# Performance work log

Measured on AMD Instinct MI355X. Metric: run time of the kernel, lower is better.

## Reference

```python
import jax, jax.numpy as jnp
import numpy as np

N = 100_000            # nodes
E = 1_600_000          # edges per metapath
IN = 256               # input features
HEADS, DIM = 8, 16     # heads * dim = hidden_channels
HIDDEN = HEADS * DIM   # 128
OUT = 4                # classes
NEG_SLOPE = 0.2


def setup_inputs() -> dict:
    key = jax.random.key(0)
    ks = jax.random.split(key, 16)
    s = 1.0 / np.sqrt(HIDDEN)
    return {
        "x": jax.random.normal(ks[0], (N, IN), jnp.float32),
        "edge_index0": jax.random.randint(ks[1], (2, E), 0, N, jnp.int64),
        "edge_index1": jax.random.randint(ks[2], (2, E), 0, N, jnp.int64),
        "proj_w": jax.random.normal(ks[3], (IN, HIDDEN), jnp.float32) / np.sqrt(IN),
        "proj_b": jnp.zeros((HIDDEN,), jnp.float32),
        "att_src0": jax.random.normal(ks[4], (HEADS, DIM), jnp.float32) * s,
        "att_dst0": jax.random.normal(ks[5], (HEADS, DIM), jnp.float32) * s,
        "att_src1": jax.random.normal(ks[6], (HEADS, DIM), jnp.float32) * s,
        "att_dst1": jax.random.normal(ks[7], (HEADS, DIM), jnp.float32) * s,
        "k_lin_w": jax.random.normal(ks[8], (HIDDEN, HIDDEN), jnp.float32) * s,
        "k_lin_b": jnp.zeros((HIDDEN,), jnp.float32),
        "q": jax.random.normal(ks[9], (HIDDEN,), jnp.float32) * s,
        "lin_w": jax.random.normal(ks[10], (HIDDEN, OUT), jnp.float32) * s,
        "lin_b": jnp.zeros((OUT,), jnp.float32),
    }


def _metapath_conv(xp, a_src, a_dst, src, dst):
    # xp: [N,H,D]; a_src, a_dst: [H,D]; src/dst: [E]
    alpha_src = (xp * a_src).sum(-1)                     # [N,H]
    alpha_dst = (xp * a_dst).sum(-1)                     # [N,H]
    e = jax.nn.leaky_relu(alpha_src[src] + alpha_dst[dst], NEG_SLOPE)  # [E,H]
    emax = jax.ops.segment_max(e, dst, num_segments=N)  # [N,H] (stable softmax)
    e = jnp.exp(e - emax[dst])
    denom = jax.ops.segment_sum(e, dst, num_segments=N)
    alpha = e / (denom[dst] + 1e-16)                     # edge softmax per dst
    msg = xp[src] * alpha[..., None]                     # [E,H,D]
    out = jax.ops.segment_sum(msg, dst, num_segments=N)  # [N,H,D]
    return jax.nn.relu(out.reshape(N, HIDDEN))


def reference(x, edge_index0, edge_index1, proj_w, proj_b,
              att_src0, att_dst0, att_src1, att_dst1,
              k_lin_w, k_lin_b, q, lin_w, lin_b):
    # shared node-type projection
    xp = (x @ proj_w + proj_b).reshape(N, HEADS, DIM)
    # per-metapath GAT-style convolutions (dropout=0.6 is eval no-op)
    outs = jnp.stack([
        _metapath_conv(xp, att_src0, att_dst0, edge_index0[0], edge_index0[1]),
        _metapath_conv(xp, att_src1, att_dst1, edge_index1[0], edge_index1[1]),
    ])                                                    # [M,N,HIDDEN]
    # semantic attention over metapaths
    k = jnp.tanh(outs @ k_lin_w + k_lin_b).mean(axis=1)  # [M,HIDDEN]
    attn = jax.nn.softmax((k * q).sum(-1))               # [M]
    fused = (attn[:, None, None] * outs).sum(0)          # [N,HIDDEN]
    return fused @ lin_w + lin_b                          # [N,OUT]
```

## Files before the change

kernel.cpp:

```cpp
#include <hip/hip_runtime.h>
#include <hip/hip_bf16.h>

#define NN 100000
#define EE 1600000
#define HID 128
#define NEG 0.2f
#define CAP 64
#define BSH 9
#define NB 196
#define CAPB 9216
#define EBLK 4096
#define NBINB 391
#define NBUILD 392
#define NPROJ 512

typedef __attribute__((ext_vector_type(8))) short short8;
typedef __attribute__((ext_vector_type(4))) float f32x4;

static __device__ __forceinline__ float bf2f(short s) {
  union { float f; unsigned u; } c;
  c.u = ((unsigned)(unsigned short)s) << 16;
  return c.f;
}

static __device__ __forceinline__ float exp2_fast(float x) {
  float r;
  asm("v_exp_f32 %0, %1" : "=v"(r) : "v"(x));
  return r;
}

static __device__ __forceinline__ float tanh_fast(float x) {
  float a = fminf(fmaxf(x * 2.885390082f, -40.f), 40.f);
  float e = exp2_fast(a);
  float r = __builtin_amdgcn_rcpf(e + 1.f);
  return fmaf(-2.f, r, 1.f);
}

__global__ __launch_bounds__(256) void k_prep(const int* __restrict__ ei0,
    const int* __restrict__ ei1, const float* __restrict__ w,
    const float* __restrict__ kw, int* __restrict__ gcur,
    int* __restrict__ binned, short* __restrict__ wTg, short* __restrict__ kwTg) {
  const int bid = blockIdx.x;
  const int t = threadIdx.x;
  if (bid >= 2 * NBINB) {
    int i = (bid - 2 * NBINB) * 256 + t;
    if (i < 32768) {
      int n = i >> 8, k = i & 255;
      __hip_bfloat16 b = __float2bfloat16(w[k * 128 + n]);
      wTg[i] = *(short*)&b;
    } else if (i < 49152) {
      int j = i - 32768;
      int n = j >> 7, k = j & 127;
      __hip_bfloat16 b = __float2bfloat16(kw[k * 128 + n]);
      kwTg[j] = *(short*)&b;
    }
    return;
  }
  const int p = bid >= NBINB;
  const int bx = p ? bid - NBINB : bid;
  const int* __restrict__ ei = p ? ei1 : ei0;
  const int* __restrict__ src = ei;
  const int* __restrict__ dst = ei + EE;
  int* __restrict__ gc = gcur + p * 256;
  int* __restrict__ bn = binned + (size_t)p * NB * CAPB;
  __shared__ int cntL[NB], baseL[NB];
  const int e0 = bx * EBLK;
  const int e1 = min(e0 + EBLK, EE);
  for (int i = t; i < NB; i += 256) cntL[i] = 0;
  __syncthreads();
  int vj[16], bj[16];
#pragma unroll
  for (int j = 0; j < 16; j++) {
    int e = e0 + t + j * 256;
    bj[j] = -1;
    if (e < e1) {
      int d = dst[e];
      int b = d >> BSH;
      int off = atomicAdd(&cntL[b], 1);
      vj[j] = (src[e] << BSH) | (d & 511);
      bj[j] = (b << 14) | off;
    }
  }
  __syncthreads();
  for (int i = t; i < NB; i += 256) baseL[i] = atomicAdd(&gc[i], cntL[i]);
  __syncthreads();
#pragma unroll
  for (int j = 0; j < 16; j++) {
    if (bj[j] >= 0) {
      int b = bj[j] >> 14;
      int off = baseL[b] + (bj[j] & 16383);
      if (off < CAPB) bn[b * CAPB + off] = vj[j];
    }
  }
}

#define PWS 264
#define PNT ((NN + 15) / 16)

__global__ __launch_bounds__(512) void k_mid(
    const int* __restrict__ gcur, const int* __restrict__ binned,
    int* __restrict__ cnt, int* __restrict__ csr,
    const float* __restrict__ x, const short* __restrict__ wTg,
    const float* __restrict__ bias,
    const float* __restrict__ a0s, const float* __restrict__ a0d,
    const float* __restrict__ a1s, const float* __restrict__ a1d,
    __hip_bfloat16* __restrict__ xph,
    float* __restrict__ as0, float* __restrict__ ad0,
    float* __restrict__ as1, float* __restrict__ ad1) {
  __shared__ short wT[128 * PWS];
  const int bid = blockIdx.x;
  const int tid = threadIdx.x;
  if (bid < NBUILD) {
    int* lc = (int*)wT;
    const int p = bid >= 196, b = p ? bid - 196 : bid;
    const int* __restrict__ bn = binned + (size_t)p * NB * CAPB + (size_t)b * CAPB;
    const int n = min(gcur[p * 256 + b], CAPB);
    int* __restrict__ cs = csr + (size_t)p * NN * CAP;
    lc[tid] = 0;
    __syncthreads();
    const int node0 = b << BSH;
    for (int i = tid; i < n; i += 512) {
      int v = bn[i];
      int ln = v & 511;
      int off = atomicAdd(&lc[ln], 1);
      if (off < CAP) cs[(size_t)(node0 + ln) * CAP + off] = v >> BSH;
    }
    __syncthreads();
    int n0 = node0 + tid;
    if (n0 < NN) cnt[p * NN + n0] = lc[tid];
    return;
  }
  const int pb = bid - NBUILD;
  for (int i = tid; i < 4096; i += 512) {
    int n = i >> 5, kc = i & 31;
    *(short8*)&wT[n * PWS + kc * 8] = *(const short8*)&wTg[n * 256 + kc * 8];
  }
  const int lane = tid & 63, wave = tid >> 6;
  const int rowgrp = lane >> 4, lcol = lane & 15;
  const bool b3 = (lcol & 8) != 0, b2 = (lcol & 4) != 0;
  const int ttype = (lcol >> 2) & 3;
  float* __restrict__ ap = (ttype == 0) ? as0 : (ttype == 1) ? ad0
                         : (ttype == 2) ? as1 : ad1;
  float bv[8], AS0[8], AD0[8], AS1[8], AD1[8];
  const float L2E = 1.44269504f;
#pragma unroll
  for (int ct = 0; ct < 8; ct++) {
    bv[ct] = bias[ct * 16 + lcol];
    AS0[ct] = a0s[ct * 16 + lcol] * L2E;
    AD0[ct] = a0d[ct * 16 + lcol] * L2E;
    AS1[ct] = a1s[ct * 16 + lcol] * L2E;
    AD1[ct] = a1d[ct * 16 + lcol] * L2E;
  }
  __syncthreads();
  for (int tile = pb * 8 + wave; tile < PNT; tile += NPROJ * 8) {
    const int r0 = tile * 16;
    int row = r0 + lcol;
    if (row >= NN) row = NN - 1;
    const float* xr = x + (size_t)row * 256 + rowgrp * 8;
    short8 af[8];
#pragma unroll
    for (int kc = 0; kc < 8; kc++) {
      float4 u0 = *(const float4*)(xr + kc * 32);
      float4 u1 = *(const float4*)(xr + kc * 32 + 4);
      union { short8 v; __hip_bfloat162 h[4]; } u;
      u.h[0] = __float22bfloat162_rn(make_float2(u0.x, u0.y));
      u.h[1] = __float22bfloat162_rn(make_float2(u0.z, u0.w));
      u.h[2] = __float22bfloat162_rn(make_float2(u1.x, u1.y));
      u.h[3] = __float22bfloat162_rn(make_float2(u1.z, u1.w));
      af[kc] = u.v;
    }
#pragma unroll
    for (int ct = 0; ct < 8; ct++) {
      f32x4 acc = {0.f, 0.f, 0.f, 0.f};
#pragma unroll
      for (int kc = 0; kc < 8; kc++) {
        short8 bf = *(const short8*)&wT[(ct * 16 + lcol) * PWS + kc * 32 + rowgrp * 8];
        acc = __builtin_amdgcn_mfma_f32_16x16x32_bf16(af[kc], bf, acc, 0, 0, 0);
      }
#pragma unroll
      for (int r = 0; r < 4; r++) {
        int orow = r0 + rowgrp * 4 + r;
        float xv = acc[r] + bv[ct];
        if (orow < NN) {
          __hip_bfloat16 ob = __float2bfloat16(xv);
          ((short*)xph)[(size_t)orow * 128 + ct * 16 + lcol] = *(short*)&ob;
        }
        float q0 = xv * AS0[ct], q1 = xv * AD0[ct], q2 = xv * AS1[ct], q3 = xv * AD1[ct];
        float va = (b3 ? q2 : q0) + __shfl_xor(b3 ? q0 : q2, 8, 64);
        float vb = (b3 ? q3 : q1) + __shfl_xor(b3 ? q1 : q3, 8, 64);
        float v  = (b2 ? vb : va) + __shfl_xor(b2 ? va : vb, 4, 64);
        v += __shfl_xor(v, 2, 64);
        v += __shfl_xor(v, 1, 64);
        if ((lcol & 3) == 0 && orow < NN) ap[orow * 8 + ct] = v;
      }
    }
  }
}


#define EDGE_BODY(sv)                                      \
  {                                                        \
    unsigned s = (unsigned)(sv);                           \
    float t = asrc[s * 8u + h];                            \
    __hip_bfloat162 v = xph[s * 64u + lane];               \
    float tt = t + ad;                                     \
    float al = exp2_fast(fmaxf(tt, NEG * tt));             \
    denom += al;                                           \
    float2 f = __bfloat1622float2(v);                      \
    a0 = fmaf(al, f.x, a0);                                \
    a1 = fmaf(al, f.y, a1);                                \
  }

__global__ __launch_bounds__(256) void k_aggr(const __hip_bfloat162* __restrict__ xph,
    const float* __restrict__ as0, const float* __restrict__ ad0,
    const float* __restrict__ as1, const float* __restrict__ ad1,
    const int* __restrict__ cnt, const int* __restrict__ csr,
    __hip_bfloat162* __restrict__ h0, __hip_bfloat162* __restrict__ h1) {
  const int p = blockIdx.y;
  const unsigned lane = threadIdx.x & 63;
  int node = blockIdx.x * 4 + (threadIdx.x >> 6);
  if (node >= NN) return;
  node = __builtin_amdgcn_readfirstlane(node);
  const float* __restrict__ asrc = p ? as1 : as0;
  const float* __restrict__ adst = p ? ad1 : ad0;
  const int* __restrict__ cs = csr + ((size_t)p * NN + node) * CAP;
  __hip_bfloat162* __restrict__ hout = p ? h1 : h0;
  const unsigned h = lane >> 3;
  const float ad = adst[(unsigned)node * 8u + h];
  const int deg = min(cnt[p * NN + node], CAP);

  float denom = 1e-16f, a0 = 0.f, a1 = 0.f;
  int e = 0;
  for (; e + 8 <= deg; e += 8) {
    int4 q0 = *(const int4*)&cs[e];
    int4 q1 = *(const int4*)&cs[e + 4];
    EDGE_BODY(q0.x) EDGE_BODY(q0.y) EDGE_BODY(q0.z) EDGE_BODY(q0.w)
    EDGE_BODY(q1.x) EDGE_BODY(q1.y) EDGE_BODY(q1.z) EDGE_BODY(q1.w)
  }
  for (; e + 4 <= deg; e += 4) {
    int4 q0 = *(const int4*)&cs[e];
    EDGE_BODY(q0.x) EDGE_BODY(q0.y) EDGE_BODY(q0.z) EDGE_BODY(q0.w)
  }
  for (; e < deg; e++) EDGE_BODY(cs[e])
  float inv = 1.f / denom;
  hout[(size_t)node * 64 + lane] =
      __float22bfloat162_rn(make_float2(fmaxf(a0 * inv, 0.f), fmaxf(a1 * inv, 0.f)));
}

#define KWS 136
#define NTILES ((NN + 63) / 64)
#define SEMGX 512

__global__ __launch_bounds__(256) void k_sem(const __hip_bfloat16* __restrict__ h0,
    const __hip_bfloat16* __restrict__ h1, const short* __restrict__ kwTg,
    const float* __restrict__ kb, const float* __restrict__ lw,
    float* __restrict__ ksum, float* __restrict__ o0, float* __restrict__ o1) {
  __shared__ short kwT[128 * KWS];
  __shared__ float red[4][128];
  __shared__ float lwS[512];
  const int tid = threadIdx.x;
  const int m = blockIdx.y;
  const short* __restrict__ hc = (const short*)(m ? h1 : h0);
  float* __restrict__ oc = m ? o1 : o0;
  for (int i = tid; i < 2048; i += 256) {
    int n = i >> 4, kc = i & 15;
    *(short8*)&kwT[n * KWS + kc * 8] = *(const short8*)&kwTg[n * 128 + kc * 8];
  }
  for (int l = tid; l < 512; l += 256) lwS[l] = lw[l];
  const int lane = tid & 63;
  const int wave = tid >> 6;
  const int rowgrp = lane >> 4;
  const int lcol = lane & 15;
  float partial[8] = {};
  float kbv[8];
#pragma unroll
  for (int ct = 0; ct < 8; ct++) kbv[ct] = kb[ct * 16 + lcol];
  __syncthreads();
  for (int tile = blockIdx.x; tile < NTILES; tile += SEMGX) {
    int n0 = tile * 64 + wave * 16;
    int row = n0 + lcol;
    if (row >= NN) row = 0;
    const short* hr = hc + (size_t)row * 128 + rowgrp * 8;
    short8 afrag[4];
#pragma unroll
    for (int kc = 0; kc < 4; kc++) afrag[kc] = *(const short8*)(hr + kc * 32);
    float op[4] = {0.f, 0.f, 0.f, 0.f};
#pragma unroll
    for (int kc = 0; kc < 4; kc++) {
      union { short8 v; short s[8]; } u;
      u.v = afrag[kc];
#pragma unroll
      for (int j = 0; j < 8; j++) {
        float hv = bf2f(u.s[j]);
        const float4 lv = *(const float4*)&lwS[(kc * 32 + rowgrp * 8 + j) * 4];
        op[0] = fmaf(hv, lv.x, op[0]);
        op[1] = fmaf(hv, lv.y, op[1]);
        op[2] = fmaf(hv, lv.z, op[2]);
        op[3] = fmaf(hv, lv.w, op[3]);
      }
    }
#pragma unroll
    for (int c = 0; c < 4; c++) {
      op[c] += __shfl_xor(op[c], 16, 64);
      op[c] += __shfl_xor(op[c], 32, 64);
    }
    int orow = n0 + lcol;
    if (rowgrp == 0 && orow < NN) {
      float4 ov = make_float4(op[0], op[1], op[2], op[3]);
      *(float4*)&oc[(size_t)orow * 4] = ov;
    }
#pragma unroll
    for (int ct = 0; ct < 8; ct++) {
      f32x4 acc = {0.f, 0.f, 0.f, 0.f};
#pragma unroll
      for (int kc = 0; kc < 4; kc++) {
        short8 bfrag = *(const short8*)&kwT[(ct * 16 + lcol) * KWS + kc * 32 + rowgrp * 8];
        acc = __builtin_amdgcn_mfma_f32_16x16x32_bf16(afrag[kc], bfrag, acc, 0, 0, 0);
      }
#pragma unroll
      for (int r = 0; r < 4; r++) {
        int node = n0 + rowgrp * 4 + r;
        if (node < NN) partial[ct] += tanh_fast(acc[r] + kbv[ct]);
      }
    }
  }
#pragma unroll
  for (int ct = 0; ct < 8; ct++) {
    partial[ct] += __shfl_xor(partial[ct], 16, 64);
    partial[ct] += __shfl_xor(partial[ct], 32, 64);
  }
  if (lane < 16) {
#pragma unroll
    for (int ct = 0; ct < 8; ct++) red[wave][ct * 16 + lane] = partial[ct];
  }
  __syncthreads();
  if (tid < 128) {
    float s = red[0][tid] + red[1][tid] + red[2][tid] + red[3][tid];
    atomicAdd(&ksum[m * 128 + tid], s);
  }
}

__global__ __launch_bounds__(256) void k_blend(const float* __restrict__ o0,
    const float* __restrict__ o1, const float* __restrict__ lb,
    const float* __restrict__ ksum, const float* __restrict__ q,
    float* __restrict__ out) {
  __shared__ float aw[2];
  const int t = threadIdx.x;
  if (t < 64) {
    float qa = q[t], qb = q[t + 64];
    float s0 = fmaf(ksum[t], qa, ksum[t + 64] * qb);
    float s1 = fmaf(ksum[128 + t], qa, ksum[192 + t] * qb);
#pragma unroll
    for (int off = 1; off < 64; off <<= 1) {
      s0 += __shfl_xor(s0, off, 64);
      s1 += __shfl_xor(s1, off, 64);
    }
    if (t == 0) {
      float l0 = s0 * (1.f / NN), l1 = s1 * (1.f / NN);
      float mx = fmaxf(l0, l1);
      float e0 = __expf(l0 - mx), e1 = __expf(l1 - mx);
      float inv = 1.f / (e0 + e1);
      aw[0] = e0 * inv;
      aw[1] = e1 * inv;
    }
  }
  __syncthreads();
  int i = blockIdx.x * 256 + t;
  if (i < NN * 4)
    out[i] = aw[0] * o0[i] + aw[1] * o1[i] + lb[i & 3];
}

extern "C" void kernel_launch(void* const* d_in, const int* in_sizes, int n_in,
                              void* d_out, int out_size, void* d_ws, size_t ws_size,
                              hipStream_t stream) {
  const float* x      = (const float*)d_in[0];
  const int*   ei0    = (const int*)d_in[1];
  const int*   ei1    = (const int*)d_in[2];
  const float* proj_w = (const float*)d_in[3];
  const float* proj_b = (const float*)d_in[4];
  const float* a0s    = (const float*)d_in[5];
  const float* a0d    = (const float*)d_in[6];
  const float* a1s    = (const float*)d_in[7];
  const float* a1d    = (const float*)d_in[8];
  const float* klw    = (const float*)d_in[9];
  const float* klb    = (const float*)d_in[10];
  const float* q      = (const float*)d_in[11];
  const float* lw     = (const float*)d_in[12];
  const float* lb     = (const float*)d_in[13];
  float* out = (float*)d_out;

  char* ws = (char*)d_ws;
  size_t off = 0;
  auto alloc = [&](size_t bytes) -> void* {
    size_t o = (off + 255) & ~(size_t)255;
    off = o + bytes;
    return (void*)(ws + o);
  };
  __hip_bfloat162* xph = (__hip_bfloat162*)alloc((size_t)NN * 128 * 2);
  __hip_bfloat162* h0  = (__hip_bfloat162*)alloc((size_t)NN * 128 * 2);
  __hip_bfloat162* h1  = (__hip_bfloat162*)alloc((size_t)NN * 128 * 2);
  float* as0  = (float*)alloc((size_t)NN * 8 * 4);
  float* ad0  = (float*)alloc((size_t)NN * 8 * 4);
  float* as1  = (float*)alloc((size_t)NN * 8 * 4);
  float* ad1  = (float*)alloc((size_t)NN * 8 * 4);
  float* ksum = (float*)alloc(256 * 4);
  int* gcur   = (int*)alloc(2 * 256 * 4);
  int* cnt    = (int*)alloc((size_t)2 * NN * 4);
  int* csr    = (int*)alloc((size_t)2 * NN * CAP * 4);
  int* binned = (int*)alloc((size_t)2 * NB * CAPB * 4);
  short* wTg  = (short*)alloc(32768 * 2);
  short* kwTg = (short*)alloc(16384 * 2);
  float* o0   = (float*)alloc((size_t)NN * 4 * 4);
  float* o1   = (float*)alloc((size_t)NN * 4 * 4);

  hipMemsetAsync(ksum, 0, 256 * 4 + 2 * 256 * 4, stream);

  k_prep<<<dim3(2 * NBINB + 192), 256, 0, stream>>>(ei0, ei1, proj_w, klw,
                                                    gcur, binned, wTg, kwTg);
  k_mid<<<dim3(NBUILD + NPROJ), 512, 0, stream>>>(gcur, binned, cnt, csr,
                                                  x, wTg, proj_b,
                                                  a0s, a0d, a1s, a1d,
                                                  (__hip_bfloat16*)xph,
                                                  as0, ad0, as1, ad1);
  k_aggr<<<dim3((NN + 3) / 4, 2), 256, 0, stream>>>(xph, as0, ad0, as1, ad1,
                                                    cnt, csr, h0, h1);
  k_sem<<<dim3(SEMGX, 2), 256, 0, stream>>>((const __hip_bfloat16*)h0,
                                            (const __hip_bfloat16*)h1, kwTg, klb, lw,
                                            ksum, o0, o1);
  k_blend<<<dim3((NN * 4 + 255) / 256), 256, 0, stream>>>(o0, o1, lb, ksum, q, out);
}
```

Baseline: 531.3 us.

## Compute attention logits with MFMA and merge them into one interleaved buffer

The per-head source and destination attention logits were computed with scalar multiplies and a shuffle reduction tree. They are now a second small bf16 MFMA against a precomputed block-diagonal weight matrix. That matrix is built in k_prep with log2(e) folded in, and the MFMA reads the just-written projected features back from global memory. The four separate logit arrays are replaced by one [N,32] buffer that k_aggr indexes per metapath. This removes shuffle and VALU work from the projection kernel. In exchange, logits are now computed from bf16-rounded features, and correctness relies on same-wave global store-then-load ordering.

```diff
diff --git a/kernel.cpp b/kernel.cpp
--- a/kernel.cpp
+++ b/kernel.cpp
@@ -13,6 +13,7 @@
 #define NBINB 391
 #define NBUILD 392
 #define NPROJ 512
+#define NPREPW 208
 
 typedef __attribute__((ext_vector_type(8))) short short8;
 typedef __attribute__((ext_vector_type(4))) float f32x4;
@@ -38,8 +39,11 @@
 
 __global__ __launch_bounds__(256) void k_prep(const int* __restrict__ ei0,
     const int* __restrict__ ei1, const float* __restrict__ w,
-    const float* __restrict__ kw, int* __restrict__ gcur,
-    int* __restrict__ binned, short* __restrict__ wTg, short* __restrict__ kwTg) {
+    const float* __restrict__ kw,
+    const float* __restrict__ a0s, const float* __restrict__ a0d,
+    const float* __restrict__ a1s, const float* __restrict__ a1d,
+    int* __restrict__ gcur, int* __restrict__ binned,
+    short* __restrict__ wTg, short* __restrict__ kwTg, short* __restrict__ awTg) {
   const int bid = blockIdx.x;
   const int t = threadIdx.x;
   if (bid >= 2 * NBINB) {
@@ -53,6 +57,14 @@
       int n = j >> 7, k = j & 127;
       __hip_bfloat16 b = __float2bfloat16(kw[k * 128 + n]);
       kwTg[j] = *(short*)&b;
+    } else if (i < 53248) {
+      int j = i - 49152;
+      int c = j >> 7, k = j & 127;
+      int p = c >> 4, dt = (c >> 3) & 1, h = c & 7;
+      const float* arr = p ? (dt ? a1d : a1s) : (dt ? a0d : a0s);
+      float v = ((k >> 4) == h) ? arr[h * 16 + (k & 15)] * 1.44269504f : 0.f;
+      __hip_bfloat16 b = __float2bfloat16(v);
+      awTg[j] = *(short*)&b;
     }
     return;
   }
@@ -95,19 +107,17 @@
 }
 
 #define PWS 264
+#define AWS 136
 #define PNT ((NN + 15) / 16)
 
 __global__ __launch_bounds__(512) void k_mid(
     const int* __restrict__ gcur, const int* __restrict__ binned,
     int* __restrict__ cnt, int* __restrict__ csr,
     const float* __restrict__ x, const short* __restrict__ wTg,
-    const float* __restrict__ bias,
-    const float* __restrict__ a0s, const float* __restrict__ a0d,
-    const float* __restrict__ a1s, const float* __restrict__ a1d,
-    __hip_bfloat16* __restrict__ xph,
-    float* __restrict__ as0, float* __restrict__ ad0,
-    float* __restrict__ as1, float* __restrict__ ad1) {
+    const short* __restrict__ awTg, const float* __restrict__ bias,
+    __hip_bfloat16* __restrict__ xph, float* __restrict__ alpha) {
   __shared__ short wT[128 * PWS];
+  __shared__ short awT[32 * AWS];
   const int bid = blockIdx.x;
   const int tid = threadIdx.x;
   if (bid < NBUILD) {
@@ -135,28 +145,20 @@
     int n = i >> 5, kc = i & 31;
     *(short8*)&wT[n * PWS + kc * 8] = *(const short8*)&wTg[n * 256 + kc * 8];
   }
+  {
+    int n = tid >> 4, kc = tid & 15;
+    *(short8*)&awT[n * AWS + kc * 8] = *(const short8*)&awTg[n * 128 + kc * 8];
+  }
   const int lane = tid & 63, wave = tid >> 6;
   const int rowgrp = lane >> 4, lcol = lane & 15;
-  const bool b3 = (lcol & 8) != 0, b2 = (lcol & 4) != 0;
-  const int ttype = (lcol >> 2) & 3;
-  float* __restrict__ ap = (ttype == 0) ? as0 : (ttype == 1) ? ad0
-                         : (ttype == 2) ? as1 : ad1;
-  float bv[8], AS0[8], AD0[8], AS1[8], AD1[8];
-  const float L2E = 1.44269504f;
-#pragma unroll
-  for (int ct = 0; ct < 8; ct++) {
-    bv[ct] = bias[ct * 16 + lcol];
-    AS0[ct] = a0s[ct * 16 + lcol] * L2E;
-    AD0[ct] = a0d[ct * 16 + lcol] * L2E;
-    AS1[ct] = a1s[ct * 16 + lcol] * L2E;
-    AD1[ct] = a1d[ct * 16 + lcol] * L2E;
-  }
-  __syncthreads();
+  float bv[8];
+#pragma unroll
+  for (int ct = 0; ct < 8; ct++) bv[ct] = bias[ct * 16 + lcol];
+  __syncthreads();
+  short* __restrict__ xphS = (short*)xph;
   for (int tile = pb * 8 + wave; tile < PNT; tile += NPROJ * 8) {
     const int r0 = tile * 16;
-    int row = r0 + lcol;
-    if (row >= NN) row = NN - 1;
-    const float* xr = x + (size_t)row * 256 + rowgrp * 8;
+    const float* xr = x + (size_t)(r0 + lcol) * 256 + rowgrp * 8;
     short8 af[8];
 #pragma unroll
     for (int kc = 0; kc < 8; kc++) {
@@ -180,19 +182,25 @@
 #pragma unroll
       for (int r = 0; r < 4; r++) {
         int orow = r0 + rowgrp * 4 + r;
-        float xv = acc[r] + bv[ct];
-        if (orow < NN) {
-          __hip_bfloat16 ob = __float2bfloat16(xv);
-          ((short*)xph)[(size_t)orow * 128 + ct * 16 + lcol] = *(short*)&ob;
-        }
-        float q0 = xv * AS0[ct], q1 = xv * AD0[ct], q2 = xv * AS1[ct], q3 = xv * AD1[ct];
-        float va = (b3 ? q2 : q0) + __shfl_xor(b3 ? q0 : q2, 8, 64);
-        float vb = (b3 ? q3 : q1) + __shfl_xor(b3 ? q1 : q3, 8, 64);
-        float v  = (b2 ? vb : va) + __shfl_xor(b2 ? va : vb, 4, 64);
-        v += __shfl_xor(v, 2, 64);
-        v += __shfl_xor(v, 1, 64);
-        if ((lcol & 3) == 0 && orow < NN) ap[orow * 8 + ct] = v;
-      }
+        __hip_bfloat16 ob = __float2bfloat16(acc[r] + bv[ct]);
+        xphS[(size_t)orow * 128 + ct * 16 + lcol] = *(short*)&ob;
+      }
+    }
+    const short* xb = xphS + (size_t)(r0 + lcol) * 128 + rowgrp * 8;
+    short8 af2[4];
+#pragma unroll
+    for (int kc = 0; kc < 4; kc++) af2[kc] = *(const short8*)(xb + kc * 32);
+#pragma unroll
+    for (int ct2 = 0; ct2 < 2; ct2++) {
+      f32x4 acc2 = {0.f, 0.f, 0.f, 0.f};
+#pragma unroll
+      for (int kc = 0; kc < 4; kc++) {
+        short8 bfa = *(const short8*)&awT[(ct2 * 16 + lcol) * AWS + kc * 32 + rowgrp * 8];
+        acc2 = __builtin_amdgcn_mfma_f32_16x16x32_bf16(af2[kc], bfa, acc2, 0, 0, 0);
+      }
+#pragma unroll
+      for (int r = 0; r < 4; r++)
+        alpha[(size_t)(r0 + rowgrp * 4 + r) * 32 + ct2 * 16 + lcol] = acc2[r];
     }
   }
 }
@@ -201,7 +209,7 @@
 #define EDGE_BODY(sv)                                      \
   {                                                        \
     unsigned s = (unsigned)(sv);                           \
-    float t = asrc[s * 8u + h];                            \
+    float t = alpha[s * 32u + pofs + h];                   \
     __hip_bfloat162 v = xph[s * 64u + lane];               \
     float tt = t + ad;                                     \
     float al = exp2_fast(fmaxf(tt, NEG * tt));             \
@@ -212,8 +220,7 @@
   }
 
 __global__ __launch_bounds__(256) void k_aggr(const __hip_bfloat162* __restrict__ xph,
-    const float* __restrict__ as0, const float* __restrict__ ad0,
-    const float* __restrict__ as1, const float* __restrict__ ad1,
+    const float* __restrict__ alpha,
     const int* __restrict__ cnt, const int* __restrict__ csr,
     __hip_bfloat162* __restrict__ h0, __hip_bfloat162* __restrict__ h1) {
   const int p = blockIdx.y;
@@ -221,12 +228,11 @@
   int node = blockIdx.x * 4 + (threadIdx.x >> 6);
   if (node >= NN) return;
   node = __builtin_amdgcn_readfirstlane(node);
-  const float* __restrict__ asrc = p ? as1 : as0;
-  const float* __restrict__ adst = p ? ad1 : ad0;
   const int* __restrict__ cs = csr + ((size_t)p * NN + node) * CAP;
   __hip_bfloat162* __restrict__ hout = p ? h1 : h0;
   const unsigned h = lane >> 3;
-  const float ad = adst[(unsigned)node * 8u + h];
+  const unsigned pofs = p * 16u;
+  const float ad = alpha[(unsigned)node * 32u + pofs + 8u + h];
   const int deg = min(cnt[p * NN + node], CAP);
 
   float denom = 1e-16f, a0 = 0.f, a1 = 0.f;
@@ -399,10 +405,7 @@
   __hip_bfloat162* xph = (__hip_bfloat162*)alloc((size_t)NN * 128 * 2);
   __hip_bfloat162* h0  = (__hip_bfloat162*)alloc((size_t)NN * 128 * 2);
   __hip_bfloat162* h1  = (__hip_bfloat162*)alloc((size_t)NN * 128 * 2);
-  float* as0  = (float*)alloc((size_t)NN * 8 * 4);
-  float* ad0  = (float*)alloc((size_t)NN * 8 * 4);
-  float* as1  = (float*)alloc((size_t)NN * 8 * 4);
-  float* ad1  = (float*)alloc((size_t)NN * 8 * 4);
+  float* alpha = (float*)alloc((size_t)NN * 32 * 4);
   float* ksum = (float*)alloc(256 * 4);
   int* gcur   = (int*)alloc(2 * 256 * 4);
   int* cnt    = (int*)alloc((size_t)2 * NN * 4);
@@ -410,20 +413,19 @@
   int* binned = (int*)alloc((size_t)2 * NB * CAPB * 4);
   short* wTg  = (short*)alloc(32768 * 2);
   short* kwTg = (short*)alloc(16384 * 2);
+  short* awTg = (short*)alloc(4096 * 2);
   float* o0   = (float*)alloc((size_t)NN * 4 * 4);
   float* o1   = (float*)alloc((size_t)NN * 4 * 4);
 
   hipMemsetAsync(ksum, 0, 256 * 4 + 2 * 256 * 4, stream);
 
-  k_prep<<<dim3(2 * NBINB + 192), 256, 0, stream>>>(ei0, ei1, proj_w, klw,
-                                                    gcur, binned, wTg, kwTg);
+  k_prep<<<dim3(2 * NBINB + NPREPW), 256, 0, stream>>>(ei0, ei1, proj_w, klw,
+                                                       a0s, a0d, a1s, a1d,
+                                                       gcur, binned, wTg, kwTg, awTg);
   k_mid<<<dim3(NBUILD + NPROJ), 512, 0, stream>>>(gcur, binned, cnt, csr,
-                                                  x, wTg, proj_b,
-                                                  a0s, a0d, a1s, a1d,
-                                                  (__hip_bfloat16*)xph,
-                                                  as0, ad0, as1, ad1);
-  k_aggr<<<dim3((NN + 3) / 4, 2), 256, 0, stream>>>(xph, as0, ad0, as1, ad1,
-                                                    cnt, csr, h0, h1);
+                                                  x, wTg, awTg, proj_b,
+                                                  (__hip_bfloat16*)xph, alpha);
+  k_aggr<<<dim3((NN + 3) / 4, 2), 256, 0, stream>>>(xph, alpha, cnt, csr, h0, h1);
   k_sem<<<dim3(SEMGX, 2), 256, 0, stream>>>((const __hip_bfloat16*)h0,
                                             (const __hip_bfloat16*)h1, kwTg, klb, lw,
                                             ksum, o0, o1);
```

Measured after the change: 534.6 us. No clear change (+0.6%).
